# Performance work log

Measured on AMD Instinct MI355X. Metric: run time of the kernel, lower is better.

Reference implementation:

```python
import jax, jax.numpy as jnp
import numpy as np

DIM = 96          # adapter bottleneck dim
K = 3             # conv kernel size

def quick_gelu(x):
    return x * jax.nn.sigmoid(1.702 * x)

def setup_inputs() -> dict:
    key = jax.random.key(0)
    ks = jax.random.split(key, 12)
    B, H, W, C = 64, 28, 28, 384
    x   = jax.random.normal(ks[0], (B, H, W, C), jnp.float32)
    # adapter down/up (xavier-ish scale for down; up is zero-init in the
    # original but we use small random so gradients flow in tests)
    Wd  = jax.random.normal(ks[1], (C, DIM), jnp.float32) * 0.05
    bd  = jnp.zeros((DIM,), jnp.float32)
    Wu  = jax.random.normal(ks[2], (DIM, C), jnp.float32) * 0.02
    bu  = jnp.zeros((C,), jnp.float32)
    # meta_net: Linear(C,64) -> ReLU -> Linear(64,64)
    Wm1 = jax.random.normal(ks[3], (C, 64), jnp.float32) * 0.05
    bm1 = jnp.zeros((64,), jnp.float32)
    Wm2 = jax.random.normal(ks[4], (64, 64), jnp.float32) * 0.1
    bm2 = jnp.zeros((64,), jnp.float32)
    # conv hypernet: Linear(64, DIM*DIM*K*K)
    Wh  = jax.random.normal(ks[5], (64, DIM * DIM * K * K), jnp.float32) * 0.01
    bh  = jnp.zeros((DIM * DIM * K * K,), jnp.float32)
    # learned layer embedding
    emb = jax.random.normal(ks[6], (64,), jnp.float32)
    return {"x": x, "Wd": Wd, "bd": bd, "Wm1": Wm1, "bm1": bm1,
            "Wm2": Wm2, "bm2": bm2, "Wh": Wh, "bh": bh, "emb": emb,
            "Wu": Wu, "bu": bu}

def reference(x, Wd, bd, Wm1, bm1, Wm2, bm2, Wh, bh, emb, Wu, bu):
    B, H, W, C = x.shape
    # meta_net(x) then mean over spatial dims -> per-sample prompt feature [B,64]
    h = jax.nn.relu(jnp.einsum('bhwc,cd->bhwd', x, Wm1) + bm1)
    prompt = jnp.mean(jnp.einsum('bhwd,de->bhwe', h, Wm2) + bm2, axis=(1, 2))  # [B,64]
    # hypernet: per-sample dynamic conv weights (fuse_type='add')
    wflat = (emb[None, :] + prompt) @ Wh + bh                 # [B, DIM*DIM*9]
    wconv = wflat.reshape(B * DIM, DIM, K, K)                 # grouped OIHW
    # adapter down + QuickGELU
    xd = quick_gelu(jnp.einsum('bhwc,cd->bhwd', x, Wd) + bd)  # [B,H,W,DIM]
    # fused batched dynamic conv via grouped conv (groups = B)
    xg = xd.transpose(0, 3, 1, 2).reshape(1, B * DIM, H, W)   # [1,B*DIM,H,W]
    yg = jax.lax.conv_general_dilated(
        xg, wconv, window_strides=(1, 1), padding=((1, 1), (1, 1)),
        dimension_numbers=('NCHW', 'OIHW', 'NCHW'), feature_group_count=B)
    y = yg.reshape(B, DIM, H, W).transpose(0, 2, 3, 1)        # [B,H,W,DIM]
    y = quick_gelu(y)  # dropout is identity in eval mode
    return jnp.einsum('bhwd,dc->bhwc', y, Wu) + bu
```

## Files before the change

kernel.cpp:

```cpp
#include <hip/hip_runtime.h>
#include <hip/hip_fp16.h>

#define BATCH 64
#define HH    28
#define WW2   28
#define HWPX  784
#define PTOT  50176
#define CIN   384
#define DIM   96
#define MDIM  64
#define JTOT  82944
#define WSAMP 82944

#define XD_OFF 0u
#define Y_OFF  9633792u
#define WP_OFF 19267584u
#define HS_OFF 29884416u
#define Z_OFF  29900800u
#define WUT_OFF 29917184u

typedef _Float16 f16x8 __attribute__((ext_vector_type(8)));
typedef _Float16 f16x4 __attribute__((ext_vector_type(4)));
typedef float f32x4 __attribute__((ext_vector_type(4)));

__device__ __forceinline__ float qgelu(float v) {
    return v / (1.f + __expf(-1.702f * v));
}

__global__ void k0_wcvt(const float* __restrict__ Wm1,
                        const float* __restrict__ Wd,
                        const float* __restrict__ Wu,
                        _Float16* __restrict__ Wt,
                        _Float16* __restrict__ WuT)
{
    int i = blockIdx.x * 256 + threadIdx.x;
    if (i < 61440) {
        int o = i / CIN, k = i - o * CIN;
        float v = (o < MDIM) ? Wm1[k * MDIM + o] : Wd[k * DIM + (o - MDIM)];
        Wt[i] = (_Float16)v;
    } else {
        int j = i - 61440;
        int c = j / DIM, d = j - c * DIM;
        WuT[j] = (_Float16)Wu[d * CIN + c];
    }
}

__global__ __launch_bounds__(512, 2) void k1_mfma(
    const float* __restrict__ x, const _Float16* __restrict__ Wt,
    const float* __restrict__ bm1, const float* __restrict__ bd,
    float* __restrict__ hsum, __half* __restrict__ xd)
{
    __shared__ char smem[46592];
    _Float16* As  = (_Float16*)smem;
    _Float16* Bs  = (_Float16*)(smem + 20480);
    float*   hred = (float*)(smem + 46080);
    _Float16* xds = (_Float16*)smem;

    const int t = threadIdx.x;
    const int p0 = blockIdx.x * 128;
    const int lane = t & 63, w = t >> 6;
    const int wm = w >> 1, wn = w & 1;
    const int rl = lane & 15, q = lane >> 4;

    const int ar0 = t >> 3, aq0 = t & 7;
    const int br0 = t >> 2, bq0 = t & 3;

    const float*    ag0 = x + (size_t)(p0 + ar0) * CIN + aq0 * 4;
    const float*    ag1 = ag0 + (size_t)64 * CIN;
    const _Float16* bg0 = Wt + br0 * CIN + bq0 * 8;
    const _Float16* bg1 = Wt + (br0 + 128) * CIN + bq0 * 8;

    float4 ra[2][2];
    uint4  rb[2][2];

#define LOADC(s, kc_) do {                                        \
    ra[s][0] = *(const float4*)(ag0 + (kc_) * 32);                \
    ra[s][1] = *(const float4*)(ag1 + (kc_) * 32);                \
    rb[s][0] = *(const uint4*)(bg0 + (kc_) * 32);                 \
    if (t < 128) rb[s][1] = *(const uint4*)(bg1 + (kc_) * 32);    \
} while (0)

#define WRITEC(buf, s) do {                                       \
    f16x4 h0, h1;                                                 \
    h0[0] = (_Float16)ra[s][0].x; h0[1] = (_Float16)ra[s][0].y;   \
    h0[2] = (_Float16)ra[s][0].z; h0[3] = (_Float16)ra[s][0].w;   \
    h1[0] = (_Float16)ra[s][1].x; h1[1] = (_Float16)ra[s][1].y;   \
    h1[2] = (_Float16)ra[s][1].z; h1[3] = (_Float16)ra[s][1].w;   \
    *(f16x4*)(As + (buf) * 5120 + ar0 * 40 + aq0 * 4) = h0;       \
    *(f16x4*)(As + (buf) * 5120 + (ar0 + 64) * 40 + aq0 * 4) = h1;\
    *(uint4*)(Bs + (buf) * 6400 + br0 * 40 + bq0 * 8) = rb[s][0]; \
    if (t < 128)                                                  \
        *(uint4*)(Bs + (buf) * 6400 + (br0 + 128) * 40 + bq0 * 8) = rb[s][1]; \
} while (0)

    f32x4 acc[2][5];
    #pragma unroll
    for (int mf = 0; mf < 2; ++mf)
        #pragma unroll
        for (int nf = 0; nf < 5; ++nf) acc[mf][nf] = (f32x4){0.f, 0.f, 0.f, 0.f};

    LOADC(0, 0);
    LOADC(1, 1);
    WRITEC(0, 0);
    __syncthreads();

    #pragma unroll
    for (int kc = 0; kc < 12; ++kc) {
        const int cur = kc & 1;

        f16x8 av[2], bv[5];
        av[0] = *(f16x8*)(As + cur * 5120 + (wm * 32 + rl) * 40 + q * 8);
        av[1] = *(f16x8*)(As + cur * 5120 + (wm * 32 + 16 + rl) * 40 + q * 8);
        #pragma unroll
        for (int nf = 0; nf < 5; ++nf)
            bv[nf] = *(f16x8*)(Bs + cur * 6400 + (wn * 80 + nf * 16 + rl) * 40 + q * 8);

        if (kc + 2 < 12) LOADC(kc & 1, kc + 2);

        #pragma unroll
        for (int mf = 0; mf < 2; ++mf)
            #pragma unroll
            for (int nf = 0; nf < 5; ++nf)
                acc[mf][nf] = __builtin_amdgcn_mfma_f32_16x16x32_f16(
                    av[mf], bv[nf], acc[mf][nf], 0, 0, 0);

        if (kc + 1 < 12) {
            WRITEC(cur ^ 1, (kc + 1) & 1);
            __syncthreads();
        }
    }
#undef LOADC
#undef WRITEC

    if (t < 128) hred[t] = 0.f;
    __syncthreads();

    const int s0 = p0 / HWPX, s_last = (p0 + 127) / HWPX;
    #pragma unroll
    for (int mf = 0; mf < 2; ++mf) {
        #pragma unroll
        for (int nf = 0; nf < 5; ++nf) {
            const int col = wn * 80 + nf * 16 + rl;
            #pragma unroll
            for (int j = 0; j < 4; ++j) {
                const int rr = wm * 32 + mf * 16 + q * 4 + j;
                float v = acc[mf][nf][j];
                if (col < 64) {
                    v = fmaxf(v + bm1[col], 0.f);
                    int sloc = (p0 + rr) / HWPX - s0;
                    atomicAdd(&hred[sloc * 64 + col], v);
                } else {
                    int e = col - 64;
                    xds[rr * 96 + e] = (_Float16)qgelu(v + bd[e]);
                }
            }
        }
    }
    __syncthreads();

    if (t < 128) {
        int sloc = t >> 6, col = t & 63, s = s0 + sloc;
        if (s <= s_last) atomicAdd(&hsum[s * 64 + col], hred[t]);
    }
    #pragma unroll
    for (int i = 0; i < 3; ++i) {
        int e = t + i * 512;
        *(uint4*)((__half*)xd + (size_t)p0 * 96 + e * 8) = *(uint4*)(xds + e * 8);
    }
}

__global__ void k2a_prompt(const float* __restrict__ hsum,
                           const float* __restrict__ Wm2,
                           const float* __restrict__ bm2,
                           const float* __restrict__ emb,
                           float* __restrict__ z)
{
    int idx = blockIdx.x * 256 + threadIdx.x;
    int b = idx >> 6, m = idx & 63;
    float acc = 0.f;
    #pragma unroll 8
    for (int d = 0; d < 64; ++d) acc += hsum[b * 64 + d] * Wm2[d * 64 + m];
    z[idx] = emb[m] + acc * (1.f / 784.f) + bm2[m];
}

__global__ __launch_bounds__(256) void k2b_hyper(
    const float* __restrict__ z, const float* __restrict__ Wh,
    const float* __restrict__ bh, __half* __restrict__ wperm)
{
    __shared__ float zs[4096];
    const int t = threadIdx.x;
    for (int idx = t; idx < 4096; idx += 256) zs[idx] = z[idx];
    const int j = blockIdx.x * 256 + t;
    float wh[64];
    #pragma unroll 8
    for (int m = 0; m < 64; ++m) wh[m] = Wh[(size_t)m * JTOT + j];
    __syncthreads();

    const int o = j / 864, rem = j % 864;
    const int i = rem / 9, t9 = rem % 9;
    const int base = o * 864 + t9 * 96 + i;
    const float bj = bh[j];
    for (int b = 0; b < 64; ++b) {
        float a = bj;
        const float4* zz = (const float4*)(zs + b * 64);
        #pragma unroll
        for (int m4 = 0; m4 < 16; ++m4) {
            float4 v = zz[m4];
            a += v.x * wh[4 * m4] + v.y * wh[4 * m4 + 1] +
                 v.z * wh[4 * m4 + 2] + v.w * wh[4 * m4 + 3];
        }
        wperm[(size_t)b * WSAMP + base] = __float2half(a);
    }
}

__global__ __launch_bounds__(256) void k3_mfma(
    const __half* __restrict__ xd, const __half* __restrict__ wperm,
    __half* __restrict__ y)
{
    __shared__ __half sm[17600];
    const int t = threadIdx.x;

    const int n = blockIdx.x;
    const int xcd = n & 7, jj0 = n >> 3;
    const int b = xcd * 8 + jj0 / 7;
    const int rt = jj0 % 7;
    const int h0 = rt * 4;

    if (t < 16) *(uint4*)(sm + 17472 + t * 8) = uint4{0u, 0u, 0u, 0u};
    for (int idx = t; idx < 2016; idx += 256) {
        int pix = idx / 12, q = idx - pix * 12;
        int r = pix / 28, col = pix - r * 28;
        int g = h0 - 1 + r;
        uint4 v = {0u, 0u, 0u, 0u};
        if ((unsigned)g < 28u)
            v = *(const uint4*)(xd + (size_t)(b * HWPX + g * 28 + col) * 96 + q * 8);
        *(uint4*)(sm + pix * 104 + q * 8) = v;
    }
    __syncthreads();

    const int lane = t & 63, w = t >> 6;
    const int wm = w >> 1, wn = w & 1;
    const int mloc = lane & 15, klo = (lane >> 4) * 8;
    const int base_m = wm * 64;

    int oh_[4], ow_[4]; bool pv[4];
    #pragma unroll
    for (int mf = 0; mf < 4; ++mf) {
        int p = base_m + mf * 16 + mloc;
        pv[mf] = (p < 112);
        int pp = pv[mf] ? p : 0;
        oh_[mf] = pp / 28; ow_[mf] = pp - oh_[mf] * 28;
    }
    const __half* wp = wperm + (size_t)b * WSAMP + (wn * 48 + mloc) * 864 + klo;

    f32x4 acc[4][3];
    #pragma unroll
    for (int mf = 0; mf < 4; ++mf)
        #pragma unroll
        for (int nf = 0; nf < 3; ++nf) acc[mf][nf] = (f32x4){0.f, 0.f, 0.f, 0.f};

    #pragma unroll
    for (int kh = 0; kh < 3; ++kh) {
        #pragma unroll
        for (int kw = 0; kw < 3; ++kw) {
            const int t9 = kh * 3 + kw;
            int abase[4];
            #pragma unroll
            for (int mf = 0; mf < 4; ++mf) {
                int iw = ow_[mf] + kw - 1;
                bool valid = pv[mf] && ((unsigned)iw < 28u);
                abase[mf] = valid ? ((oh_[mf] + kh) * 28 + iw) * 104 + klo
                                  : 17472 + klo;
            }
            #pragma unroll
            for (int ic = 0; ic < 3; ++ic) {
                f16x8 av[4], bv[3];
                #pragma unroll
                for (int nf = 0; nf < 3; ++nf)
                    bv[nf] = *(const f16x8*)(wp + nf * 13824 + t9 * 96 + ic * 32);
                #pragma unroll
                for (int mf = 0; mf < 4; ++mf)
                    av[mf] = *(const f16x8*)(sm + abase[mf] + ic * 32);
                #pragma unroll
                for (int mf = 0; mf < 4; ++mf)
                    #pragma unroll
                    for (int nf = 0; nf < 3; ++nf)
                        acc[mf][nf] = __builtin_amdgcn_mfma_f32_16x16x32_f16(
                            av[mf], bv[nf], acc[mf][nf], 0, 0, 0);
            }
        }
    }
    __syncthreads();

    #pragma unroll
    for (int mf = 0; mf < 4; ++mf) {
        #pragma unroll
        for (int nf = 0; nf < 3; ++nf) {
            const int o = wn * 48 + nf * 16 + mloc;
            #pragma unroll
            for (int j = 0; j < 4; ++j) {
                int p = base_m + mf * 16 + (lane >> 4) * 4 + j;
                if (p < 112)
                    sm[p * 104 + o] = __float2half(qgelu(acc[mf][nf][j]));
            }
        }
    }
    __syncthreads();
    for (int idx = t; idx < 1344; idx += 256) {
        int pix = idx / 12, q = idx - pix * 12;
        *(uint4*)(y + (size_t)(b * HWPX + h0 * 28 + pix) * 96 + q * 8) =
            *(uint4*)(sm + pix * 104 + q * 8);
    }
}

__global__ __launch_bounds__(512, 2) void k4_mfma(
    const __half* __restrict__ y, const _Float16* __restrict__ WuT,
    const float* __restrict__ bu, float* __restrict__ out)
{
    __shared__ __half ys[128 * 104];
    const int t = threadIdx.x;
    const int p0 = blockIdx.x * 128;

    #pragma unroll
    for (int i = 0; i < 3; ++i) {
        int idx = t + i * 512;
        int pix = idx / 12, q = idx - pix * 12;
        *(uint4*)(ys + pix * 104 + q * 8) =
            *(const uint4*)(y + (size_t)(p0 + pix) * 96 + q * 8);
    }

    const int lane = t & 63, w = t >> 6;
    const int wm = w >> 2, wn = w & 3;
    const int mloc = lane & 15, klo = (lane >> 4) * 8;

    float bcol[6];
    #pragma unroll
    for (int nf = 0; nf < 6; ++nf) bcol[nf] = bu[wn * 96 + nf * 16 + mloc];
    __syncthreads();

    f32x4 acc[4][6];
    #pragma unroll
    for (int mf = 0; mf < 4; ++mf)
        #pragma unroll
        for (int nf = 0; nf < 6; ++nf) acc[mf][nf] = (f32x4){0.f, 0.f, 0.f, 0.f};

    #pragma unroll
    for (int kc = 0; kc < 3; ++kc) {
        f16x8 av[4], bv[6];
        #pragma unroll
        for (int nf = 0; nf < 6; ++nf)
            bv[nf] = *(const f16x8*)(WuT + (wn * 96 + nf * 16 + mloc) * 96 + kc * 32 + klo);
        #pragma unroll
        for (int mf = 0; mf < 4; ++mf)
            av[mf] = *(const f16x8*)(ys + (wm * 64 + mf * 16 + mloc) * 104 + kc * 32 + klo);
        #pragma unroll
        for (int mf = 0; mf < 4; ++mf)
            #pragma unroll
            for (int nf = 0; nf < 6; ++nf)
                acc[mf][nf] = __builtin_amdgcn_mfma_f32_16x16x32_f16(
                    av[mf], bv[nf], acc[mf][nf], 0, 0, 0);
    }

    #pragma unroll
    for (int mf = 0; mf < 4; ++mf) {
        #pragma unroll
        for (int nf = 0; nf < 6; ++nf) {
            const int c = wn * 96 + nf * 16 + mloc;
            #pragma unroll
            for (int j = 0; j < 4; ++j) {
                int p = p0 + wm * 64 + mf * 16 + (lane >> 4) * 4 + j;
                out[(size_t)p * CIN + c] = acc[mf][nf][j] + bcol[nf];
            }
        }
    }
}

extern "C" void kernel_launch(void* const* d_in, const int* in_sizes, int n_in,
                              void* d_out, int out_size, void* d_ws, size_t ws_size,
                              hipStream_t stream)
{
    const float* x   = (const float*)d_in[0];
    const float* Wd  = (const float*)d_in[1];
    const float* bd  = (const float*)d_in[2];
    const float* Wm1 = (const float*)d_in[3];
    const float* bm1 = (const float*)d_in[4];
    const float* Wm2 = (const float*)d_in[5];
    const float* bm2 = (const float*)d_in[6];
    const float* Wh  = (const float*)d_in[7];
    const float* bh  = (const float*)d_in[8];
    const float* emb = (const float*)d_in[9];
    const float* Wu  = (const float*)d_in[10];
    const float* bu  = (const float*)d_in[11];
    float* out = (float*)d_out;

    char* ws = (char*)d_ws;
    __half*   xd    = (__half*)(ws + XD_OFF);
    __half*   ybuf  = (__half*)(ws + Y_OFF);
    __half*   wperm = (__half*)(ws + WP_OFF);
    float*    hsum  = (float*)(ws + HS_OFF);
    float*    z     = (float*)(ws + Z_OFF);
    _Float16* Wt    = (_Float16*)(ws + WP_OFF);
    _Float16* WuT   = (_Float16*)(ws + WUT_OFF);

    hipMemsetAsync(hsum, 0, 64 * 64 * sizeof(float), stream);

    k0_wcvt<<<384, 256, 0, stream>>>(Wm1, Wd, Wu, Wt, WuT);
    k1_mfma<<<392, 512, 0, stream>>>(x, Wt, bm1, bd, hsum, xd);
    k2a_prompt<<<16, 256, 0, stream>>>(hsum, Wm2, bm2, emb, z);
    k2b_hyper<<<324, 256, 0, stream>>>(z, Wh, bh, wperm);
    k3_mfma<<<448, 256, 0, stream>>>(xd, wperm, ybuf);
    k4_mfma<<<392, 512, 0, stream>>>(ybuf, WuT, bu, out);
}
```

Baseline: 151.1 us.

## Stage hypernet outputs in LDS for coalesced writes; use lighter barriers in k1

The hypernet kernel now assigns each block a quarter of one output channel's 864 weights. It computes them into shared memory in the permuted (tap, input) order, then writes contiguous 8-byte chunks to wperm instead of scattered 2-byte stores. This uses 384 blocks with 216 active threads each, leaving some lanes idle during compute. In k1, __syncthreads is replaced by an LDS-only waitcnt plus s_barrier, which avoids waiting on outstanding global prefetch loads at each k-step. An extra full barrier is added before the reduction buffer is reset.

```diff
diff --git a/kernel.cpp b/kernel.cpp
--- a/kernel.cpp
+++ b/kernel.cpp
@@ -93,6 +93,11 @@
         *(uint4*)(Bs + (buf) * 6400 + (br0 + 128) * 40 + bq0 * 8) = rb[s][1]; \
 } while (0)
 
+#define SOFT_BARRIER() do {                                       \
+    asm volatile("s_waitcnt lgkmcnt(0)" ::: "memory");            \
+    __builtin_amdgcn_s_barrier();                                 \
+} while (0)
+
     f32x4 acc[2][5];
     #pragma unroll
     for (int mf = 0; mf < 2; ++mf)
@@ -102,7 +107,7 @@
     LOADC(0, 0);
     LOADC(1, 1);
     WRITEC(0, 0);
-    __syncthreads();
+    SOFT_BARRIER();
 
     #pragma unroll
     for (int kc = 0; kc < 12; ++kc) {
@@ -115,7 +120,7 @@
         for (int nf = 0; nf < 5; ++nf)
             bv[nf] = *(f16x8*)(Bs + cur * 6400 + (wn * 80 + nf * 16 + rl) * 40 + q * 8);
 
-        if (kc + 2 < 12) LOADC(kc & 1, kc + 2);
+        if (kc + 2 < 12) LOADC(cur, kc + 2);
 
         #pragma unroll
         for (int mf = 0; mf < 2; ++mf)
@@ -125,13 +130,15 @@
                     av[mf], bv[nf], acc[mf][nf], 0, 0, 0);
 
         if (kc + 1 < 12) {
-            WRITEC(cur ^ 1, (kc + 1) & 1);
-            __syncthreads();
+            WRITEC(cur ^ 1, cur ^ 1);
+            SOFT_BARRIER();
         }
     }
 #undef LOADC
 #undef WRITEC
-
+#undef SOFT_BARRIER
+
+    __syncthreads();
     if (t < 128) hred[t] = 0.f;
     __syncthreads();
 
@@ -187,29 +194,46 @@
     const float* __restrict__ z, const float* __restrict__ Wh,
     const float* __restrict__ bh, __half* __restrict__ wperm)
 {
-    __shared__ float zs[4096];
+    __shared__ float  zs[4096];
+    __shared__ __half wl[64 * 216];
     const int t = threadIdx.x;
+    const int o = blockIdx.x >> 2, qd = blockIdx.x & 3;
+
     for (int idx = t; idx < 4096; idx += 256) zs[idx] = z[idx];
-    const int j = blockIdx.x * 256 + t;
+
+    const bool act = (t < 216);
+    const int j = o * 864 + qd * 216 + (act ? t : 0);
     float wh[64];
-    #pragma unroll 8
-    for (int m = 0; m < 64; ++m) wh[m] = Wh[(size_t)m * JTOT + j];
-    __syncthreads();
-
-    const int o = j / 864, rem = j % 864;
-    const int i = rem / 9, t9 = rem % 9;
-    const int base = o * 864 + t9 * 96 + i;
-    const float bj = bh[j];
-    for (int b = 0; b < 64; ++b) {
-        float a = bj;
-        const float4* zz = (const float4*)(zs + b * 64);
-        #pragma unroll
-        for (int m4 = 0; m4 < 16; ++m4) {
-            float4 v = zz[m4];
-            a += v.x * wh[4 * m4] + v.y * wh[4 * m4 + 1] +
-                 v.z * wh[4 * m4 + 2] + v.w * wh[4 * m4 + 3];
-        }
-        wperm[(size_t)b * WSAMP + base] = __float2half(a);
+    float bj = 0.f;
+    if (act) {
+        #pragma unroll 8
+        for (int m = 0; m < 64; ++m) wh[m] = Wh[(size_t)m * JTOT + j];
+        bj = bh[j];
+    }
+    __syncthreads();
+
+    if (act) {
+        const int il = t / 9, t9 = t - il * 9;
+        const int loc = t9 * 24 + il;
+        for (int b = 0; b < 64; ++b) {
+            float a = bj;
+            const float4* zz = (const float4*)(zs + b * 64);
+            #pragma unroll
+            for (int m4 = 0; m4 < 16; ++m4) {
+                float4 v = zz[m4];
+                a += v.x * wh[4 * m4] + v.y * wh[4 * m4 + 1] +
+                     v.z * wh[4 * m4 + 2] + v.w * wh[4 * m4 + 3];
+            }
+            wl[b * 216 + loc] = __float2half(a);
+        }
+    }
+    __syncthreads();
+
+    for (int idx = t; idx < 3456; idx += 256) {
+        int b = idx / 54, r = idx - b * 54;
+        int t9 = r / 6, il4 = r - t9 * 6;
+        *(uint2*)(wperm + (size_t)b * WSAMP + o * 864 + t9 * 96 + qd * 24 + il4 * 4) =
+            *(const uint2*)(wl + b * 216 + t9 * 24 + il4 * 4);
     }
 }
 
@@ -407,7 +431,7 @@
     k0_wcvt<<<384, 256, 0, stream>>>(Wm1, Wd, Wu, Wt, WuT);
     k1_mfma<<<392, 512, 0, stream>>>(x, Wt, bm1, bd, hsum, xd);
     k2a_prompt<<<16, 256, 0, stream>>>(hsum, Wm2, bm2, emb, z);
-    k2b_hyper<<<324, 256, 0, stream>>>(z, Wh, bh, wperm);
+    k2b_hyper<<<384, 256, 0, stream>>>(z, Wh, bh, wperm);
     k3_mfma<<<448, 256, 0, stream>>>(xd, wperm, ybuf);
     k4_mfma<<<392, 512, 0, stream>>>(ybuf, WuT, bu, out);
 }
```

Result: no change. 150.2 us (-0.6%).
